# Optimization experiments

Hardware: AMD Instinct MI355X
Metric: run time of the kernel (lower is better)

The kernel has to match this reference:

```python
import jax, jax.numpy as jnp
import numpy as np

B, DZ, M_, N_ = 2048, 256, 64, 64
GAMMA, EPS, MAXITERS = 1.0, 1e-6, 1000


def sinkhorn(Mcost):
    # entropic OT with uniform marginals r=1/m, c=1/n (ddn sinkhorn, non-logspace)
    b, h, w = Mcost.shape
    r = 1.0 / h
    c = 1.0 / w
    P = jnp.exp(-GAMMA * Mcost)
    P = P / jnp.sum(P, axis=(1, 2), keepdims=True)

    def cond_fn(state):
        P, it, err = state
        return jnp.logical_and(it < MAXITERS, err > EPS)

    def body_fn(state):
        P, it, _ = state
        alpha = jnp.sum(P, axis=2, keepdims=True)   # row sums (B,h,1)
        P = P * (r / alpha)                          # row normalize to r
        beta = jnp.sum(P, axis=1, keepdims=True)    # col sums (B,1,w)
        err = jnp.max(jnp.abs(beta - c))
        # torch loop breaks BEFORE col-normalizing when converged
        P = jnp.where(err <= EPS, P, P * (c / beta))
        return P, it + 1, err

    init_err = jnp.array(jnp.inf, dtype=Mcost.dtype)
    P, _, _ = jax.lax.while_loop(cond_fn, body_fn, (P, jnp.array(0, jnp.int32), init_err))
    return P


def setup_inputs() -> dict:
    key = jax.random.key(0)
    ks = jax.random.split(key, 7)
    H = M_ * N_
    z = jax.random.normal(ks[0], (B, DZ), dtype=jnp.float32)
    W1 = jax.random.normal(ks[1], (DZ, H), dtype=jnp.float32) * (1.0 / np.sqrt(DZ))
    b1 = jnp.zeros((H,), jnp.float32)
    W2 = jax.random.normal(ks[2], (H, H), dtype=jnp.float32) * (1.0 / np.sqrt(H))
    b2 = jnp.zeros((H,), jnp.float32)
    W3 = jax.random.normal(ks[3], (H, H), dtype=jnp.float32) * (1.0 / np.sqrt(H))
    b3 = jnp.zeros((H,), jnp.float32)
    return {"z": z, "W1": W1, "b1": b1, "W2": W2, "b2": b2, "W3": W3, "b3": b3}


def reference(z, W1, b1, W2, b2, W3, b3):
    x = jax.nn.relu(z @ W1 + b1)
    x = jax.nn.relu(x @ W2 + b2)
    x = x @ W3 + b3
    x = x.reshape(z.shape[0], M_, N_)  # (B, m, n) cost matrix
    return sinkhorn(x)
```

## Files before the change

### kernel.cpp

```cpp
#include <hip/hip_runtime.h>
#include <hip/hip_bf16.h>

typedef unsigned short ushort_t;
typedef __attribute__((ext_vector_type(8))) short bf16x8;
typedef __attribute__((ext_vector_type(4))) float f32x4;

#define MDIM 2048
#define NDIM 4096

__device__ __forceinline__ ushort_t to_bf16(float f) {
    __hip_bfloat16 h = __float2bfloat16(f);
    return *reinterpret_cast<ushort_t*>(&h);
}

__global__ void cast_bf16_kernel(const float* __restrict__ in, ushort_t* __restrict__ out, int n) {
    int i = blockIdx.x * blockDim.x + threadIdx.x;
    if (i < n) out[i] = to_bf16(in[i]);
}

__global__ void transpose_cast_kernel(const float* __restrict__ W, ushort_t* __restrict__ WT,
                                      int K, int N) {
    __shared__ float tile[32][33];
    const int tx = threadIdx.x, ty = threadIdx.y;
    const int n0 = blockIdx.x * 32, k0 = blockIdx.y * 32;
#pragma unroll
    for (int r = 0; r < 4; ++r)
        tile[ty + r * 8][tx] = W[(size_t)(k0 + ty + r * 8) * N + n0 + tx];
    __syncthreads();
    const int t = ty * 32 + tx;
    const int nl = t >> 3;
    const int kc = (t & 7) * 4;
    ushort4 o;
    o.x = to_bf16(tile[kc + 0][nl]);
    o.y = to_bf16(tile[kc + 1][nl]);
    o.z = to_bf16(tile[kc + 2][nl]);
    o.w = to_bf16(tile[kc + 3][nl]);
    *reinterpret_cast<ushort4*>(&WT[(size_t)(n0 + nl) * K + k0 + kc]) = o;
}


#define GLD(gp, lp) __builtin_amdgcn_global_load_lds(                      \
        (const __attribute__((address_space(1))) void*)(gp),               \
        (__attribute__((address_space(3))) void*)(lp), 16, 0, 0)

#define MFMA(d, a, b) d = __builtin_amdgcn_mfma_f32_16x16x32_bf16(a, b, d, 0, 0, 0)

template <typename OutT, bool RELU>
__global__ __launch_bounds__(512, 2) void gemm_p8(const ushort_t* __restrict__ A,
                                                  const ushort_t* __restrict__ BT,
                                                  const float* __restrict__ bias,
                                                  OutT* __restrict__ C, int Kdim) {
    __shared__ __align__(16) ushort_t As[3][128 * 64];
    __shared__ __align__(16) ushort_t Bs[3][256 * 64];

    const int t = threadIdx.x;
    const int l = t & 63;
    const int w = t >> 6;
    const int l16 = l & 15;
    const int quad = l >> 4;
    const int wr = w >> 2;
    const int wc = w & 3;
    const int m0 = blockIdx.y * 128;
    const int n0 = blockIdx.x * 256;

    f32x4 acc[4][4];
#pragma unroll
    for (int i = 0; i < 4; ++i)
#pragma unroll
        for (int j = 0; j < 4; ++j) acc[i][j] = (f32x4){0.f, 0.f, 0.f, 0.f};

    const int srow = w * 8 + (l >> 3);
    const int scol = ((l & 7) ^ (l >> 3)) * 8;
    const ushort_t* gA0 = A  + (size_t)(m0 + srow) * Kdim + scol;
    const ushort_t* gA1 = A  + (size_t)(m0 + 64 + srow) * Kdim + scol;
    const ushort_t* gB0 = BT + (size_t)(n0 + srow) * Kdim + scol;
    const ushort_t* gB1 = BT + (size_t)(n0 + 64 + srow) * Kdim + scol;
    const ushort_t* gB2 = BT + (size_t)(n0 + 128 + srow) * Kdim + scol;
    const ushort_t* gB3 = BT + (size_t)(n0 + 192 + srow) * Kdim + scol;
    const int ldsW = w * 8 * 64;

    const int swz = l16 & 7;
#define LDA_(base, i, kk) (*(const bf16x8*)&(base)[(wr * 64 + (i) * 16 + l16) * 64 + ((((kk) * 4 + quad) ^ swz) * 8)])
#define LDB_(base, j, kk) (*(const bf16x8*)&(base)[(wc * 64 + (j) * 16 + l16) * 64 + ((((kk) * 4 + quad) ^ swz) * 8)])

#define STAGE_TILE(buf, koff) do {                      \
        GLD(gA0 + (koff), &As[buf][ldsW]);              \
        GLD(gA1 + (koff), &As[buf][ldsW + 64 * 64]);    \
        GLD(gB0 + (koff), &Bs[buf][ldsW]);              \
        GLD(gB1 + (koff), &Bs[buf][ldsW + 64 * 64]);    \
        GLD(gB2 + (koff), &Bs[buf][ldsW + 128 * 64]);   \
        GLD(gB3 + (koff), &Bs[buf][ldsW + 192 * 64]);   \
    } while (0)

#define MFMA16(a0, a1, a2, a3, b0, b1, b2, b3)                     \
        MFMA(acc[0][0], a0, b0); MFMA(acc[0][1], a0, b1);          \
        MFMA(acc[0][2], a0, b2); MFMA(acc[0][3], a0, b3);          \
        MFMA(acc[1][0], a1, b0); MFMA(acc[1][1], a1, b1);          \
        MFMA(acc[1][2], a1, b2); MFMA(acc[1][3], a1, b3);          \
        MFMA(acc[2][0], a2, b0); MFMA(acc[2][1], a2, b1);          \
        MFMA(acc[2][2], a2, b2); MFMA(acc[2][3], a2, b3);          \
        MFMA(acc[3][0], a3, b0); MFMA(acc[3][1], a3, b1);          \
        MFMA(acc[3][2], a3, b2); MFMA(acc[3][3], a3, b3)

    const int nt = Kdim >> 6;

    STAGE_TILE(0, 0);
    STAGE_TILE(1, 64);
    asm volatile("s_waitcnt vmcnt(6)" ::: "memory");
    __builtin_amdgcn_s_barrier();

    for (int tt = 0; tt < nt; ++tt) {
        const int buf = tt % 3;
        const int nb = (tt + 2) % 3;
        const int koff = (tt + 2) << 6;
        const bool more = (tt + 2) < nt;

        const ushort_t* __restrict__ Ab = &As[buf][0];
        const ushort_t* __restrict__ Bb = &Bs[buf][0];

        bf16x8 a00 = LDA_(Ab, 0, 0), a01 = LDA_(Ab, 1, 0), a02 = LDA_(Ab, 2, 0), a03 = LDA_(Ab, 3, 0);
        bf16x8 b00 = LDB_(Bb, 0, 0), b01 = LDB_(Bb, 1, 0), b02 = LDB_(Bb, 2, 0), b03 = LDB_(Bb, 3, 0);
        bf16x8 a10 = LDA_(Ab, 0, 1), a11 = LDA_(Ab, 1, 1), a12 = LDA_(Ab, 2, 1), a13 = LDA_(Ab, 3, 1);
        bf16x8 b10 = LDB_(Bb, 0, 1), b11 = LDB_(Bb, 1, 1), b12 = LDB_(Bb, 2, 1), b13 = LDB_(Bb, 3, 1);

        if (more) STAGE_TILE(nb, koff);

        MFMA16(a00, a01, a02, a03, b00, b01, b02, b03);
        MFMA16(a10, a11, a12, a13, b10, b11, b12, b13);

        if (tt + 1 < nt) {
            if (more) asm volatile("s_waitcnt vmcnt(6)" ::: "memory");
            else      asm volatile("s_waitcnt vmcnt(0)" ::: "memory");
            __builtin_amdgcn_s_barrier();
        }
    }

#pragma unroll
    for (int i = 0; i < 4; ++i) {
#pragma unroll
        for (int r = 0; r < 4; ++r) {
            const int grow = m0 + wr * 64 + i * 16 + quad * 4 + r;
#pragma unroll
            for (int j = 0; j < 4; ++j) {
                const int gcol = n0 + wc * 64 + j * 16 + l16;
                float v = acc[i][j][r] + bias[gcol];
                if (RELU) v = fmaxf(v, 0.0f);
                if constexpr (sizeof(OutT) == 2) {
                    C[(size_t)grow * NDIM + gcol] = to_bf16(v);
                } else {
                    C[(size_t)grow * NDIM + gcol] = v;
                }
            }
        }
    }
}

__device__ __forceinline__ float rdl(float v, int l) {
    return __uint_as_float(__builtin_amdgcn_readlane(__float_as_uint(v), l));
}

__global__ __launch_bounds__(64) void sinkhorn_kernel(float* __restrict__ PM) {
    __shared__ __align__(16) float T[64 * 65];
    const int l = threadIdx.x;
    float* base = PM + (size_t)blockIdx.x * 4096;

    float Kcol[64];
    float Krow[64];
#pragma unroll
    for (int r = 0; r < 64; ++r)
        Kcol[r] = __expf(-base[r * 64 + l]);
#pragma unroll
    for (int r = 0; r < 64; ++r)
        T[r * 65 + l] = Kcol[r];
    __syncthreads();
#pragma unroll
    for (int c = 0; c < 64; ++c)
        Krow[c] = T[l * 65 + c];

    float a = 0.0f, b = 1.0f;
    for (int it = 0; it < 1000; ++it) {
        float t1 = 0.0f;
#pragma unroll
        for (int c = 0; c < 64; ++c)
            t1 = fmaf(Krow[c], rdl(b, c), t1);
        a = 0.015625f / t1;

        float t2 = 0.0f;
#pragma unroll
        for (int r = 0; r < 64; ++r)
            t2 = fmaf(Kcol[r], rdl(a, r), t2);
        const float err = fabsf(b * t2 - 0.015625f);
        if (__ballot(err > 1e-6f) == 0ull) break;
        b = 0.015625f / t2;
    }

#pragma unroll
    for (int r = 0; r < 64; ++r)
        base[r * 64 + l] = rdl(a, r) * Kcol[r] * b;
}

extern "C" void kernel_launch(void* const* d_in, const int* in_sizes, int n_in,
                              void* d_out, int out_size, void* d_ws, size_t ws_size,
                              hipStream_t stream) {
    const float* z  = (const float*)d_in[0];
    const float* W1 = (const float*)d_in[1];
    const float* b1 = (const float*)d_in[2];
    const float* W2 = (const float*)d_in[3];
    const float* b2 = (const float*)d_in[4];
    const float* W3 = (const float*)d_in[5];
    const float* b3 = (const float*)d_in[6];
    float* out = (float*)d_out;
    char* ws = (char*)d_ws;

    ushort_t* W2T = (ushort_t*)(ws + 0);
    ushort_t* W3T = (ushort_t*)(ws + (size_t)33554432);
    ushort_t* C1b = (ushort_t*)(ws + (size_t)67108864);
    ushort_t* C2b = (ushort_t*)(ws + (size_t)83886080);
    ushort_t* Zb  = (ushort_t*)(ws + (size_t)100663296);
    ushort_t* W1T = (ushort_t*)(ws + (size_t)101711872);

    cast_bf16_kernel<<<2048, 256, 0, stream>>>(z, Zb, MDIM * 256);
    transpose_cast_kernel<<<dim3(128, 8), dim3(32, 8), 0, stream>>>(W1, W1T, 256, 4096);
    transpose_cast_kernel<<<dim3(128, 128), dim3(32, 8), 0, stream>>>(W2, W2T, 4096, 4096);
    transpose_cast_kernel<<<dim3(128, 128), dim3(32, 8), 0, stream>>>(W3, W3T, 4096, 4096);

    gemm_p8<ushort_t, true><<<dim3(NDIM / 256, MDIM / 128), 512, 0, stream>>>(Zb, W1T, b1, C1b, 256);
    gemm_p8<ushort_t, true><<<dim3(NDIM / 256, MDIM / 128), 512, 0, stream>>>(C1b, W2T, b2, C2b, 4096);
    gemm_p8<float, false><<<dim3(NDIM / 256, MDIM / 128), 512, 0, stream>>>(C2b, W3T, b3, out, 4096);

    sinkhorn_kernel<<<2048, 64, 0, stream>>>(out);
}
```

Measured before the change: 333.0 us.

## Load B operand directly from global into registers, bypassing LDS

The B (weight) tile is no longer staged through shared memory. Each wave loads its own B fragments straight from global memory into registers, prefetching one K-step ahead, while A stays on the triple-buffered LDS path. This cuts LDS capacity use and LDS read traffic for B, which may allow more occupancy. The cost is uncoalesced-style 16-byte per-lane global loads for B, duplicated across the waves sharing a column, and more registers held for the prefetched fragments.

```diff
diff --git a/kernel.cpp b/kernel.cpp
--- a/kernel.cpp
+++ b/kernel.cpp
@@ -51,7 +51,6 @@
                                                   const float* __restrict__ bias,
                                                   OutT* __restrict__ C, int Kdim) {
     __shared__ __align__(16) ushort_t As[3][128 * 64];
-    __shared__ __align__(16) ushort_t Bs[3][256 * 64];
 
     const int t = threadIdx.x;
     const int l = t & 63;
@@ -71,25 +70,22 @@
 
     const int srow = w * 8 + (l >> 3);
     const int scol = ((l & 7) ^ (l >> 3)) * 8;
-    const ushort_t* gA0 = A  + (size_t)(m0 + srow) * Kdim + scol;
-    const ushort_t* gA1 = A  + (size_t)(m0 + 64 + srow) * Kdim + scol;
-    const ushort_t* gB0 = BT + (size_t)(n0 + srow) * Kdim + scol;
-    const ushort_t* gB1 = BT + (size_t)(n0 + 64 + srow) * Kdim + scol;
-    const ushort_t* gB2 = BT + (size_t)(n0 + 128 + srow) * Kdim + scol;
-    const ushort_t* gB3 = BT + (size_t)(n0 + 192 + srow) * Kdim + scol;
+    const ushort_t* gA0 = A + (size_t)(m0 + srow) * Kdim + scol;
+    const ushort_t* gA1 = A + (size_t)(m0 + 64 + srow) * Kdim + scol;
     const int ldsW = w * 8 * 64;
 
     const int swz = l16 & 7;
 #define LDA_(base, i, kk) (*(const bf16x8*)&(base)[(wr * 64 + (i) * 16 + l16) * 64 + ((((kk) * 4 + quad) ^ swz) * 8)])
-#define LDB_(base, j, kk) (*(const bf16x8*)&(base)[(wc * 64 + (j) * 16 + l16) * 64 + ((((kk) * 4 + quad) ^ swz) * 8)])
-
-#define STAGE_TILE(buf, koff) do {                      \
+
+    const ushort_t* pB0 = BT + (size_t)(n0 + wc * 64 + 0 * 16 + l16) * Kdim + quad * 8;
+    const ushort_t* pB1 = BT + (size_t)(n0 + wc * 64 + 1 * 16 + l16) * Kdim + quad * 8;
+    const ushort_t* pB2 = BT + (size_t)(n0 + wc * 64 + 2 * 16 + l16) * Kdim + quad * 8;
+    const ushort_t* pB3 = BT + (size_t)(n0 + wc * 64 + 3 * 16 + l16) * Kdim + quad * 8;
+#define BL(p, kk, ttn) (*reinterpret_cast<const bf16x8*>((p) + (size_t)(ttn) * 64 + (kk) * 32))
+
+#define STAGE_A(buf, koff) do {                         \
         GLD(gA0 + (koff), &As[buf][ldsW]);              \
         GLD(gA1 + (koff), &As[buf][ldsW + 64 * 64]);    \
-        GLD(gB0 + (koff), &Bs[buf][ldsW]);              \
-        GLD(gB1 + (koff), &Bs[buf][ldsW + 64 * 64]);    \
-        GLD(gB2 + (koff), &Bs[buf][ldsW + 128 * 64]);   \
-        GLD(gB3 + (koff), &Bs[buf][ldsW + 192 * 64]);   \
     } while (0)
 
 #define MFMA16(a0, a1, a2, a3, b0, b1, b2, b3)                     \
@@ -104,34 +100,46 @@
 
     const int nt = Kdim >> 6;
 
-    STAGE_TILE(0, 0);
-    STAGE_TILE(1, 64);
-    asm volatile("s_waitcnt vmcnt(6)" ::: "memory");
+    STAGE_A(0, 0);
+    __builtin_amdgcn_sched_barrier(0);
+    bf16x8 bc00 = BL(pB0, 0, 0), bc01 = BL(pB0, 1, 0);
+    bf16x8 bc10 = BL(pB1, 0, 0), bc11 = BL(pB1, 1, 0);
+    bf16x8 bc20 = BL(pB2, 0, 0), bc21 = BL(pB2, 1, 0);
+    bf16x8 bc30 = BL(pB3, 0, 0), bc31 = BL(pB3, 1, 0);
+    __builtin_amdgcn_sched_barrier(0);
+    STAGE_A(1, 64);
+    asm volatile("s_waitcnt vmcnt(2)" ::: "memory");
     __builtin_amdgcn_s_barrier();
 
     for (int tt = 0; tt < nt; ++tt) {
         const int buf = tt % 3;
         const int nb = (tt + 2) % 3;
-        const int koff = (tt + 2) << 6;
         const bool more = (tt + 2) < nt;
 
         const ushort_t* __restrict__ Ab = &As[buf][0];
-        const ushort_t* __restrict__ Bb = &Bs[buf][0];
 
         bf16x8 a00 = LDA_(Ab, 0, 0), a01 = LDA_(Ab, 1, 0), a02 = LDA_(Ab, 2, 0), a03 = LDA_(Ab, 3, 0);
-        bf16x8 b00 = LDB_(Bb, 0, 0), b01 = LDB_(Bb, 1, 0), b02 = LDB_(Bb, 2, 0), b03 = LDB_(Bb, 3, 0);
         bf16x8 a10 = LDA_(Ab, 0, 1), a11 = LDA_(Ab, 1, 1), a12 = LDA_(Ab, 2, 1), a13 = LDA_(Ab, 3, 1);
-        bf16x8 b10 = LDB_(Bb, 0, 1), b11 = LDB_(Bb, 1, 1), b12 = LDB_(Bb, 2, 1), b13 = LDB_(Bb, 3, 1);
-
-        if (more) STAGE_TILE(nb, koff);
-
-        MFMA16(a00, a01, a02, a03, b00, b01, b02, b03);
-        MFMA16(a10, a11, a12, a13, b10, b11, b12, b13);
-
+
+        bf16x8 bn00, bn01, bn10, bn11, bn20, bn21, bn30, bn31;
         if (tt + 1 < nt) {
-            if (more) asm volatile("s_waitcnt vmcnt(6)" ::: "memory");
+            bn00 = BL(pB0, 0, tt + 1); bn01 = BL(pB0, 1, tt + 1);
+            bn10 = BL(pB1, 0, tt + 1); bn11 = BL(pB1, 1, tt + 1);
+            bn20 = BL(pB2, 0, tt + 1); bn21 = BL(pB2, 1, tt + 1);
+            bn30 = BL(pB3, 0, tt + 1); bn31 = BL(pB3, 1, tt + 1);
+        }
+        __builtin_amdgcn_sched_barrier(0);
+        if (more) STAGE_A(nb, (tt + 2) << 6);
+
+        MFMA16(a00, a01, a02, a03, bc00, bc10, bc20, bc30);
+        MFMA16(a10, a11, a12, a13, bc01, bc11, bc21, bc31);
+
+        if (tt + 1 < nt) {
+            if (more) asm volatile("s_waitcnt vmcnt(2)" ::: "memory");
             else      asm volatile("s_waitcnt vmcnt(0)" ::: "memory");
             __builtin_amdgcn_s_barrier();
+            bc00 = bn00; bc01 = bn01; bc10 = bn10; bc11 = bn11;
+            bc20 = bn20; bc21 = bn21; bc30 = bn30; bc31 = bn31;
         }
     }
 
```

Result: slower. 544.2 us (+63.4%).

## Shrink GEMM tile to 128x128 with 4 waves and double buffering

Applied to the files above, without the earlier changes.

Changes the bf16 MFMA GEMM from a 128x256 tile with 8 waves and a triple-buffered LDS pipeline to a 128x128 tile with 4 waves and double buffering. The next tile's global-to-LDS loads are now issued before the LDS reads of the current tile, and each iteration waits for all loads to finish. This doubles the grid size and cuts LDS use per block, which may raise occupancy and wave-level parallelism. In exchange each block reuses less data, so global traffic goes up, and the prefetch depth drops from two tiles to one.

```diff
diff --git a/kernel.cpp b/kernel.cpp
--- a/kernel.cpp
+++ b/kernel.cpp
@@ -46,22 +46,22 @@
 #define MFMA(d, a, b) d = __builtin_amdgcn_mfma_f32_16x16x32_bf16(a, b, d, 0, 0, 0)
 
 template <typename OutT, bool RELU>
-__global__ __launch_bounds__(512, 2) void gemm_p8(const ushort_t* __restrict__ A,
+__global__ __launch_bounds__(256, 2) void gemm_p8(const ushort_t* __restrict__ A,
                                                   const ushort_t* __restrict__ BT,
                                                   const float* __restrict__ bias,
                                                   OutT* __restrict__ C, int Kdim) {
-    __shared__ __align__(16) ushort_t As[3][128 * 64];
-    __shared__ __align__(16) ushort_t Bs[3][256 * 64];
+    __shared__ __align__(16) ushort_t As[2][128 * 64];
+    __shared__ __align__(16) ushort_t Bs[2][128 * 64];
 
     const int t = threadIdx.x;
     const int l = t & 63;
     const int w = t >> 6;
     const int l16 = l & 15;
     const int quad = l >> 4;
-    const int wr = w >> 2;
-    const int wc = w & 3;
+    const int wr = w >> 1;
+    const int wc = w & 1;
     const int m0 = blockIdx.y * 128;
-    const int n0 = blockIdx.x * 256;
+    const int n0 = blockIdx.x * 128;
 
     f32x4 acc[4][4];
 #pragma unroll
@@ -69,27 +69,26 @@
 #pragma unroll
         for (int j = 0; j < 4; ++j) acc[i][j] = (f32x4){0.f, 0.f, 0.f, 0.f};
 
-    const int srow = w * 8 + (l >> 3);
-    const int scol = ((l & 7) ^ (l >> 3)) * 8;
-    const ushort_t* gA0 = A  + (size_t)(m0 + srow) * Kdim + scol;
-    const ushort_t* gA1 = A  + (size_t)(m0 + 64 + srow) * Kdim + scol;
-    const ushort_t* gB0 = BT + (size_t)(n0 + srow) * Kdim + scol;
-    const ushort_t* gB1 = BT + (size_t)(n0 + 64 + srow) * Kdim + scol;
-    const ushort_t* gB2 = BT + (size_t)(n0 + 128 + srow) * Kdim + scol;
-    const ushort_t* gB3 = BT + (size_t)(n0 + 192 + srow) * Kdim + scol;
+    const int srow = t >> 3;
+    const int scol = ((t & 7) ^ (srow & 7)) * 8;
+    const ushort_t* gA = A  + (size_t)(m0 + srow) * Kdim + scol;
+    const ushort_t* gB = BT + (size_t)(n0 + srow) * Kdim + scol;
     const int ldsW = w * 8 * 64;
 
     const int swz = l16 & 7;
 #define LDA_(base, i, kk) (*(const bf16x8*)&(base)[(wr * 64 + (i) * 16 + l16) * 64 + ((((kk) * 4 + quad) ^ swz) * 8)])
 #define LDB_(base, j, kk) (*(const bf16x8*)&(base)[(wc * 64 + (j) * 16 + l16) * 64 + ((((kk) * 4 + quad) ^ swz) * 8)])
 
-#define STAGE_TILE(buf, koff) do {                      \
-        GLD(gA0 + (koff), &As[buf][ldsW]);              \
-        GLD(gA1 + (koff), &As[buf][ldsW + 64 * 64]);    \
-        GLD(gB0 + (koff), &Bs[buf][ldsW]);              \
-        GLD(gB1 + (koff), &Bs[buf][ldsW + 64 * 64]);    \
-        GLD(gB2 + (koff), &Bs[buf][ldsW + 128 * 64]);   \
-        GLD(gB3 + (koff), &Bs[buf][ldsW + 192 * 64]);   \
+    const size_t rstep = (size_t)32 * Kdim;
+#define STAGE_TILE(buf, koff) do {                                  \
+        GLD(gA + (koff),             &As[buf][ldsW]);               \
+        GLD(gA + (koff) + rstep,     &As[buf][ldsW + 32 * 64]);     \
+        GLD(gA + (koff) + 2 * rstep, &As[buf][ldsW + 64 * 64]);     \
+        GLD(gA + (koff) + 3 * rstep, &As[buf][ldsW + 96 * 64]);     \
+        GLD(gB + (koff),             &Bs[buf][ldsW]);               \
+        GLD(gB + (koff) + rstep,     &Bs[buf][ldsW + 32 * 64]);     \
+        GLD(gB + (koff) + 2 * rstep, &Bs[buf][ldsW + 64 * 64]);     \
+        GLD(gB + (koff) + 3 * rstep, &Bs[buf][ldsW + 96 * 64]);     \
     } while (0)
 
 #define MFMA16(a0, a1, a2, a3, b0, b1, b2, b3)                     \
@@ -105,15 +104,14 @@
     const int nt = Kdim >> 6;
 
     STAGE_TILE(0, 0);
-    STAGE_TILE(1, 64);
-    asm volatile("s_waitcnt vmcnt(6)" ::: "memory");
+    asm volatile("s_waitcnt vmcnt(0)" ::: "memory");
     __builtin_amdgcn_s_barrier();
 
     for (int tt = 0; tt < nt; ++tt) {
-        const int buf = tt % 3;
-        const int nb = (tt + 2) % 3;
-        const int koff = (tt + 2) << 6;
-        const bool more = (tt + 2) < nt;
+        const int buf = tt & 1;
+
+        if (tt + 1 < nt) STAGE_TILE(buf ^ 1, (tt + 1) << 6);
+        __builtin_amdgcn_sched_barrier(0);
 
         const ushort_t* __restrict__ Ab = &As[buf][0];
         const ushort_t* __restrict__ Bb = &Bs[buf][0];
@@ -123,14 +121,11 @@
         bf16x8 a10 = LDA_(Ab, 0, 1), a11 = LDA_(Ab, 1, 1), a12 = LDA_(Ab, 2, 1), a13 = LDA_(Ab, 3, 1);
         bf16x8 b10 = LDB_(Bb, 0, 1), b11 = LDB_(Bb, 1, 1), b12 = LDB_(Bb, 2, 1), b13 = LDB_(Bb, 3, 1);
 
-        if (more) STAGE_TILE(nb, koff);
-
         MFMA16(a00, a01, a02, a03, b00, b01, b02, b03);
         MFMA16(a10, a11, a12, a13, b10, b11, b12, b13);
 
         if (tt + 1 < nt) {
-            if (more) asm volatile("s_waitcnt vmcnt(6)" ::: "memory");
-            else      asm volatile("s_waitcnt vmcnt(0)" ::: "memory");
+            asm volatile("s_waitcnt vmcnt(0)" ::: "memory");
             __builtin_amdgcn_s_barrier();
         }
     }
@@ -224,9 +219,9 @@
     transpose_cast_kernel<<<dim3(128, 128), dim3(32, 8), 0, stream>>>(W2, W2T, 4096, 4096);
     transpose_cast_kernel<<<dim3(128, 128), dim3(32, 8), 0, stream>>>(W3, W3T, 4096, 4096);
 
-    gemm_p8<ushort_t, true><<<dim3(NDIM / 256, MDIM / 128), 512, 0, stream>>>(Zb, W1T, b1, C1b, 256);
-    gemm_p8<ushort_t, true><<<dim3(NDIM / 256, MDIM / 128), 512, 0, stream>>>(C1b, W2T, b2, C2b, 4096);
-    gemm_p8<float, false><<<dim3(NDIM / 256, MDIM / 128), 512, 0, stream>>>(C2b, W3T, b3, out, 4096);
+    gemm_p8<ushort_t, true><<<dim3(NDIM / 128, MDIM / 128), 256, 0, stream>>>(Zb, W1T, b1, C1b, 256);
+    gemm_p8<ushort_t, true><<<dim3(NDIM / 128, MDIM / 128), 256, 0, stream>>>(C1b, W2T, b2, C2b, 4096);
+    gemm_p8<float, false><<<dim3(NDIM / 128, MDIM / 128), 256, 0, stream>>>(C2b, W3T, b3, out, 4096);
 
     sinkhorn_kernel<<<2048, 64, 0, stream>>>(out);
 }
```

Result: slower. 349.8 us (+5.1%).

## Broadcast Sinkhorn scaling vectors via LDS float4 reads and pin GEMM MFMA scheduling

Applied to the files above, without the earlier changes.

The Sinkhorn loop used to broadcast each lane's scaling factor with 64 serial readlane operations. It now writes the vectors to shared memory and reads them back as float4 broadcasts, using four independent accumulators to shorten the dependency chain of FMAs. The GEMM inner loop gets sched_barriers and split lgkmcnt waits, so the first half of the MFMAs can start before all LDS fragment loads complete. The 64-thread block relies on wavefront-synchronous LDS writes and reads with no explicit barrier, and changing the summation order slightly alters rounding.

```diff
diff --git a/kernel.cpp b/kernel.cpp
--- a/kernel.cpp
+++ b/kernel.cpp
@@ -120,12 +120,20 @@
 
         bf16x8 a00 = LDA_(Ab, 0, 0), a01 = LDA_(Ab, 1, 0), a02 = LDA_(Ab, 2, 0), a03 = LDA_(Ab, 3, 0);
         bf16x8 b00 = LDB_(Bb, 0, 0), b01 = LDB_(Bb, 1, 0), b02 = LDB_(Bb, 2, 0), b03 = LDB_(Bb, 3, 0);
+        __builtin_amdgcn_sched_barrier(0);
         bf16x8 a10 = LDA_(Ab, 0, 1), a11 = LDA_(Ab, 1, 1), a12 = LDA_(Ab, 2, 1), a13 = LDA_(Ab, 3, 1);
         bf16x8 b10 = LDB_(Bb, 0, 1), b11 = LDB_(Bb, 1, 1), b12 = LDB_(Bb, 2, 1), b13 = LDB_(Bb, 3, 1);
+        __builtin_amdgcn_sched_barrier(0);
 
         if (more) STAGE_TILE(nb, koff);
-
+        __builtin_amdgcn_sched_barrier(0);
+
+        asm volatile("s_waitcnt lgkmcnt(8)" ::: "memory");
+        __builtin_amdgcn_sched_barrier(0);
         MFMA16(a00, a01, a02, a03, b00, b01, b02, b03);
+        __builtin_amdgcn_sched_barrier(0);
+        asm volatile("s_waitcnt lgkmcnt(0)" ::: "memory");
+        __builtin_amdgcn_sched_barrier(0);
         MFMA16(a10, a11, a12, a13, b10, b11, b12, b13);
 
         if (tt + 1 < nt) {
@@ -155,12 +163,10 @@
     }
 }
 
-__device__ __forceinline__ float rdl(float v, int l) {
-    return __uint_as_float(__builtin_amdgcn_readlane(__float_as_uint(v), l));
-}
-
 __global__ __launch_bounds__(64) void sinkhorn_kernel(float* __restrict__ PM) {
     __shared__ __align__(16) float T[64 * 65];
+    __shared__ __align__(16) float vecA[64];
+    __shared__ __align__(16) float vecB[64];
     const int l = threadIdx.x;
     float* base = PM + (size_t)blockIdx.x * 4096;
 
@@ -177,26 +183,54 @@
     for (int c = 0; c < 64; ++c)
         Krow[c] = T[l * 65 + c];
 
+    const float4* __restrict__ vA4 = reinterpret_cast<const float4*>(vecA);
+    const float4* __restrict__ vB4 = reinterpret_cast<const float4*>(vecB);
+
     float a = 0.0f, b = 1.0f;
     for (int it = 0; it < 1000; ++it) {
-        float t1 = 0.0f;
-#pragma unroll
-        for (int c = 0; c < 64; ++c)
-            t1 = fmaf(Krow[c], rdl(b, c), t1);
+        vecB[l] = b;
+        asm volatile("s_waitcnt lgkmcnt(0)" ::: "memory");
+        __builtin_amdgcn_sched_barrier(0);
+        float s0 = 0.f, s1 = 0.f, s2 = 0.f, s3 = 0.f;
+#pragma unroll
+        for (int q = 0; q < 16; ++q) {
+            const float4 v = vB4[q];
+            s0 = fmaf(Krow[4 * q + 0], v.x, s0);
+            s1 = fmaf(Krow[4 * q + 1], v.y, s1);
+            s2 = fmaf(Krow[4 * q + 2], v.z, s2);
+            s3 = fmaf(Krow[4 * q + 3], v.w, s3);
+        }
+        const float t1 = (s0 + s1) + (s2 + s3);
         a = 0.015625f / t1;
 
-        float t2 = 0.0f;
-#pragma unroll
-        for (int r = 0; r < 64; ++r)
-            t2 = fmaf(Kcol[r], rdl(a, r), t2);
+        vecA[l] = a;
+        asm volatile("s_waitcnt lgkmcnt(0)" ::: "memory");
+        __builtin_amdgcn_sched_barrier(0);
+        float u0 = 0.f, u1 = 0.f, u2 = 0.f, u3 = 0.f;
+#pragma unroll
+        for (int q = 0; q < 16; ++q) {
+            const float4 v = vA4[q];
+            u0 = fmaf(Kcol[4 * q + 0], v.x, u0);
+            u1 = fmaf(Kcol[4 * q + 1], v.y, u1);
+            u2 = fmaf(Kcol[4 * q + 2], v.z, u2);
+            u3 = fmaf(Kcol[4 * q + 3], v.w, u3);
+        }
+        const float t2 = (u0 + u1) + (u2 + u3);
         const float err = fabsf(b * t2 - 0.015625f);
         if (__ballot(err > 1e-6f) == 0ull) break;
         b = 0.015625f / t2;
     }
 
-#pragma unroll
-    for (int r = 0; r < 64; ++r)
-        base[r * 64 + l] = rdl(a, r) * Kcol[r] * b;
+    asm volatile("s_waitcnt lgkmcnt(0)" ::: "memory");
+    __builtin_amdgcn_sched_barrier(0);
+#pragma unroll
+    for (int q = 0; q < 16; ++q) {
+        const float4 av = vA4[q];
+        base[(4 * q + 0) * 64 + l] = av.x * Kcol[4 * q + 0] * b;
+        base[(4 * q + 1) * 64 + l] = av.y * Kcol[4 * q + 1] * b;
+        base[(4 * q + 2) * 64 + l] = av.z * Kcol[4 * q + 2] * b;
+        base[(4 * q + 3) * 64 + l] = av.w * Kcol[4 * q + 3] * b;
+    }
 }
 
 extern "C" void kernel_launch(void* const* d_in, const int* in_sizes, int n_in,
```

New measurement: 338.8 us. About the same (+1.7%).
